# Kernel tuning notes

Hardware: AMD Instinct MI355X
Metric: run time of the kernel (lower is better)

The kernel has to match this reference:

```python
import jax, jax.numpy as jnp
import numpy as np

VOCAB = 100
EMB = 256
HID = 256
B = 8
S = 2048


def setup_inputs() -> dict:
    key = jax.random.key(0)
    ks = jax.random.split(key, 12)
    s_e = 1.0 / np.sqrt(EMB)
    s_h = 1.0 / np.sqrt(HID)
    return {
        "x": jax.random.randint(ks[0], (B, S), 0, VOCAB),
        "embedding": jax.random.normal(ks[1], (VOCAB, EMB), jnp.float32),
        "w_ih": jax.random.uniform(ks[2], (3 * HID, EMB), jnp.float32, -s_e, s_e),
        "w_hh": jax.random.uniform(ks[3], (3 * HID, HID), jnp.float32, -s_h, s_h),
        "b_ih": jax.random.uniform(ks[4], (3 * HID,), jnp.float32, -s_h, s_h),
        "b_hh": jax.random.uniform(ks[5], (3 * HID,), jnp.float32, -s_h, s_h),
        "attn_w": jax.random.uniform(ks[6], (HID, HID), jnp.float32, -s_h, s_h),
        "attn_b": jax.random.uniform(ks[7], (HID,), jnp.float32, -s_h, s_h),
        "comb_w": jax.random.uniform(ks[8], (HID, 2 * HID), jnp.float32, -s_h, s_h),
        "comb_b": jax.random.uniform(ks[9], (HID,), jnp.float32, -s_h, s_h),
        "fc_w": jax.random.uniform(ks[10], (VOCAB, HID), jnp.float32, -s_h, s_h),
        "fc_b": jax.random.uniform(ks[11], (VOCAB,), jnp.float32, -s_h, s_h),
    }


def _gru(emb, w_ih, w_hh, b_ih, b_hh):
    # emb: [B, S, E]; PyTorch GRU gate order: r, z, n
    xg = jnp.einsum('bse,ge->bsg', emb, w_ih) + b_ih  # [B, S, 3H]
    h0 = jnp.zeros((emb.shape[0], HID), emb.dtype)

    def step(h, xg_t):
        hg = h @ w_hh.T + b_hh
        xr, xz, xn = jnp.split(xg_t, 3, axis=-1)
        hr, hz, hn = jnp.split(hg, 3, axis=-1)
        r = jax.nn.sigmoid(xr + hr)
        z = jax.nn.sigmoid(xz + hz)
        n = jnp.tanh(xn + r * hn)
        h_new = (1.0 - z) * n + z * h
        return h_new, h_new

    h_last, hs = jax.lax.scan(step, h0, jnp.swapaxes(xg, 0, 1))
    return jnp.swapaxes(hs, 0, 1), h_last  # [B,S,H], [B,H]


def reference(x, embedding, w_ih, w_hh, b_ih, b_hh, attn_w, attn_b, comb_w, comb_b, fc_w, fc_b):
    emb = embedding[x]  # [B, S, E]
    all_h, h_last = _gru(emb, w_ih, w_hh, b_ih, b_hh)
    keys = jnp.einsum('bsh,kh->bsk', all_h, attn_w) + attn_b  # [B,S,H]
    scores = jnp.einsum('bqh,bkh->bqk', all_h, keys)  # [B,S,S]
    seq = all_h.shape[1]
    causal = jnp.tril(jnp.ones((seq, seq), bool))
    scores = jnp.where(causal[None], scores, -jnp.inf)
    attn = jax.nn.softmax(scores, axis=-1)
    context = jnp.einsum('bqk,bkh->bqh', attn, all_h)  # [B,S,H]
    combined = jnp.concatenate([all_h, context], axis=-1)
    combined = jnp.tanh(jnp.einsum('bsd,hd->bsh', combined, comb_w) + comb_b)
    output = jnp.einsum('bsh,vh->bsv', combined, fc_w) + fc_b
    return output, h_last[None]  # hidden: [num_layers=1, B, H]
```

## Files before the change

### kernel.cpp

```cpp
#include <hip/hip_runtime.h>

#define SEQ  2048
#define NB   8
#define HD   256
#define G3   768
#define NV   100
#define KVB  32

typedef float f32x4 __attribute__((ext_vector_type(4)));
typedef int   i32x4 __attribute__((ext_vector_type(4)));
typedef short s16x8 __attribute__((ext_vector_type(8)));
typedef unsigned short u16x4 __attribute__((ext_vector_type(4)));

#define INV26 1.490116119384765625e-8f

__device__ __forceinline__ float rcp_fast(float x) {
  return __builtin_amdgcn_rcpf(x);
}
__device__ __forceinline__ float sigm(float x) {
  x = fminf(fmaxf(x, -30.f), 30.f);
  return rcp_fast(1.f + __expf(-x));
}
__device__ __forceinline__ float tanh_fast(float x) {
  x = fminf(fmaxf(x, -15.f), 15.f);
  float e = __expf(2.f * x);
  return (e - 1.f) * rcp_fast(e + 1.f);
}
__device__ __forceinline__ void cvt_hilo(float f, unsigned short& h, unsigned short& l) {
  unsigned u = __float_as_uint(f);
  h = (unsigned short)(u >> 16);
  float r = f - __uint_as_float(u & 0xffff0000u);
  l = (unsigned short)(__float_as_uint(r) >> 16);
}

__global__ __launch_bounds__(256) void build_table(
    const float* __restrict__ emb, const float* __restrict__ w_ih,
    const float* __restrict__ b_ih, float* __restrict__ table) {
  __shared__ float eL[256];
  __shared__ float wL[256][37];
  int v = blockIdx.x, tid = threadIdx.x;
  eL[tid] = emb[v * HD + tid];
  for (int gt = 0; gt < 3; ++gt) {
    float acc = b_ih[gt * 256 + tid];
    for (int e0 = 0; e0 < HD; e0 += 32) {
      __syncthreads();
      #pragma unroll
      for (int i = 0; i < 32; ++i) {
        int idx = tid + i * 256;
        int r = idx >> 5, c = idx & 31;
        wL[r][c] = w_ih[(size_t)(gt * 256 + r) * HD + e0 + c];
      }
      __syncthreads();
      #pragma unroll
      for (int c = 0; c < 32; ++c) acc += eL[e0 + c] * wL[tid][c];
    }
    table[((size_t)v * 256 + tid) * 4 + gt] = acc;
  }
}

__global__ void __launch_bounds__(512) gru_scan(
    const int* __restrict__ x, const float* __restrict__ w_hh,
    const float* __restrict__ b_hh, const float* __restrict__ table,
    float* __restrict__ all_h, float* __restrict__ h_last) {
  __shared__ __align__(16) signed char hpk[2][2 * 272];
  __shared__ int xs[SEQ];
  const int b = blockIdx.x;
  int tid = threadIdx.x;
  int lane = tid & 63, wv = tid >> 6;
  int ncol = lane & 15, quad = lane >> 4;
  int usel = quad & 1;
  int j = wv * 32 + usel * 16 + ncol;

  for (int i = tid; i < SEQ; i += 512) xs[i] = x[b * SEQ + i];
  for (int i = tid; i < 2 * 272; i += 512)
    hpk[0][i] = (i >= 272) ? (signed char)-128 : 0;

  i32x4 bw[2][3][4];
  float Cn2[2][3];
  #pragma unroll
  for (int u = 0; u < 2; ++u) {
    #pragma unroll
    for (int t3 = 0; t3 < 3; ++t3) {
      int row = t3 * 256 + wv * 32 + u * 16 + ncol;
      int sw = 0;
      #pragma unroll
      for (int c = 0; c < 4; ++c) {
        const float* p = w_hh + (size_t)row * HD + c * 64 + quad * 16;
        unsigned pw[4] = {0u, 0u, 0u, 0u};
        #pragma unroll
        for (int e = 0; e < 16; ++e) {
          int q = __float2int_rn(p[e] * 2048.f);
          q = max(-127, min(127, q));
          sw += q;
          pw[e >> 2] |= ((unsigned)(q & 255)) << ((e & 3) * 8);
        }
        bw[u][t3][c] = (i32x4){(int)pw[0], (int)pw[1], (int)pw[2], (int)pw[3]};
      }
      sw += __shfl_xor(sw, 16);
      sw += __shfl_xor(sw, 32);
      Cn2[u][t3] = b_hh[row] + 128.f * (float)sw * INV26;
    }
  }
  float Csel[3];
  #pragma unroll
  for (int t3 = 0; t3 < 3; ++t3) Csel[t3] = usel ? Cn2[1][t3] : Cn2[0][t3];

  float hreg = 0.f;
  __syncthreads();
  float xr, xz, xn;
  {
    int v = xs[0];
    f32x4 xg = *(const f32x4*)&table[((size_t)v * 256 + j) * 4];
    xr = xg[0]; xz = xg[1]; xn = xg[2];
  }
  int a_base = (ncol & 1) * 272 + quad * 16;

  for (int t = 0; t < SEQ; ++t) {
    const signed char* cb = hpk[t & 1];
    i32x4 a[4];
    #pragma unroll
    for (int c = 0; c < 4; ++c)
      a[c] = *(const i32x4*)&cb[a_base + c * 64];
    float hg[3];
    #pragma unroll
    for (int t3 = 0; t3 < 3; ++t3) {
      i32x4 A0 = {0, 0, 0, 0}, A1 = {0, 0, 0, 0};
      #pragma unroll
      for (int c = 0; c < 4; ++c) {
        A0 = __builtin_amdgcn_mfma_i32_16x16x64_i8(a[c], bw[0][t3][c], A0, 0, 0, 0);
        A1 = __builtin_amdgcn_mfma_i32_16x16x64_i8(a[c], bw[1][t3][c], A1, 0, 0, 0);
      }
      int d0 = usel ? A1[0] : A0[0];
      int d1 = usel ? A1[1] : A0[1];
      hg[t3] = ((float)d0 * 256.f + (float)d1) * INV26 + Csel[t3];
    }
    float r = sigm(xr + hg[0]);
    float z = sigm(xz + hg[1]);
    float n = tanh_fast(xn + r * hg[2]);
    float h = (1.f - z) * n + z * hreg;
    hreg = h;
    int q = min(__float2int_rn(h * 32768.f), 32767);
    int lou = q & 255;
    int hi8 = (q - lou) >> 8;
    signed char* nx = hpk[(t + 1) & 1];
    if (quad < 2) {
      nx[j] = (signed char)hi8;
      nx[272 + j] = (signed char)(lou - 128);
      all_h[((size_t)b * SEQ + t) * HD + j] = h;
    }
    int v = xs[(t + 1 < SEQ) ? t + 1 : t];
    f32x4 xg = *(const f32x4*)&table[((size_t)v * 256 + j) * 4];
    xr = xg[0]; xz = xg[1]; xn = xg[2];
    __syncthreads();
  }
  if (quad < 2) h_last[b * HD + j] = hreg;
}

template<int ACT>
__global__ __launch_bounds__(256) void gemm_bias(
    const float* __restrict__ A, int lda,
    const float* __restrict__ W, const float* __restrict__ bias,
    float* __restrict__ C, int ldc, int N, int K) {
  __shared__ float As[128][36];
  __shared__ float Ws[64][36];
  int tid = threadIdx.x;
  int m0 = blockIdx.y * 128, n0 = blockIdx.x * 64;
  int ml = tid & 31, g = tid >> 5;
  float acc[4][8];
  #pragma unroll
  for (int i = 0; i < 4; ++i)
    #pragma unroll
    for (int jj = 0; jj < 8; ++jj) acc[i][jj] = 0.f;
  for (int k0 = 0; k0 < K; k0 += 32) {
    __syncthreads();
    #pragma unroll
    for (int i = 0; i < 4; ++i) {
      int idx = tid + i * 256;
      int r = idx >> 3, c4 = (idx & 7) * 4;
      *(f32x4*)&As[r][c4] = *(const f32x4*)&A[(size_t)(m0 + r) * lda + k0 + c4];
    }
    #pragma unroll
    for (int i = 0; i < 2; ++i) {
      int idx = tid + i * 256;
      int r = idx >> 3, c4 = (idx & 7) * 4;
      f32x4 wv = {0.f, 0.f, 0.f, 0.f};
      if (n0 + r < N) wv = *(const f32x4*)&W[(size_t)(n0 + r) * K + k0 + c4];
      *(f32x4*)&Ws[r][c4] = wv;
    }
    __syncthreads();
    #pragma unroll
    for (int k4 = 0; k4 < 32; k4 += 4) {
      f32x4 av[4], wv8[8];
      #pragma unroll
      for (int i = 0; i < 4; ++i) av[i] = *(const f32x4*)&As[ml + i * 32][k4];
      #pragma unroll
      for (int jj = 0; jj < 8; ++jj) wv8[jj] = *(const f32x4*)&Ws[g * 8 + jj][k4];
      #pragma unroll
      for (int kk = 0; kk < 4; ++kk)
        #pragma unroll
        for (int i = 0; i < 4; ++i)
          #pragma unroll
          for (int jj = 0; jj < 8; ++jj)
            acc[i][jj] += av[i][kk] * wv8[jj][kk];
    }
  }
  #pragma unroll
  for (int i = 0; i < 4; ++i) {
    int m = m0 + ml + i * 32;
    #pragma unroll
    for (int jj = 0; jj < 8; ++jj) {
      int n = n0 + g * 8 + jj;
      if (n < N) {
        float val = acc[i][jj] + bias[n];
        if (ACT) val = tanh_fast(val);
        C[(size_t)m * ldc + n] = val;
      }
    }
  }
}

__global__ __launch_bounds__(256) void gemm_bias_cat(
    const float* __restrict__ A1, const float* __restrict__ A2,
    const float* __restrict__ W, const float* __restrict__ bias,
    float* __restrict__ C) {
  __shared__ float As[128][36];
  __shared__ float Ws[64][36];
  const int K = 512;
  int tid = threadIdx.x;
  int m0 = blockIdx.y * 128, n0 = blockIdx.x * 64;
  int ml = tid & 31, g = tid >> 5;
  float acc[4][8];
  #pragma unroll
  for (int i = 0; i < 4; ++i)
    #pragma unroll
    for (int jj = 0; jj < 8; ++jj) acc[i][jj] = 0.f;
  for (int k0 = 0; k0 < K; k0 += 32) {
    const float* src = (k0 < 256) ? A1 : A2;
    int kb = (k0 < 256) ? k0 : k0 - 256;
    __syncthreads();
    #pragma unroll
    for (int i = 0; i < 4; ++i) {
      int idx = tid + i * 256;
      int r = idx >> 3, c4 = (idx & 7) * 4;
      *(f32x4*)&As[r][c4] = *(const f32x4*)&src[(size_t)(m0 + r) * 256 + kb + c4];
    }
    #pragma unroll
    for (int i = 0; i < 2; ++i) {
      int idx = tid + i * 256;
      int r = idx >> 3, c4 = (idx & 7) * 4;
      *(f32x4*)&Ws[r][c4] = *(const f32x4*)&W[(size_t)(n0 + r) * K + k0 + c4];
    }
    __syncthreads();
    #pragma unroll
    for (int k4 = 0; k4 < 32; k4 += 4) {
      f32x4 av[4], wv8[8];
      #pragma unroll
      for (int i = 0; i < 4; ++i) av[i] = *(const f32x4*)&As[ml + i * 32][k4];
      #pragma unroll
      for (int jj = 0; jj < 8; ++jj) wv8[jj] = *(const f32x4*)&Ws[g * 8 + jj][k4];
      #pragma unroll
      for (int kk = 0; kk < 4; ++kk)
        #pragma unroll
        for (int i = 0; i < 4; ++i)
          #pragma unroll
          for (int jj = 0; jj < 8; ++jj)
            acc[i][jj] += av[i][kk] * wv8[jj][kk];
    }
  }
  #pragma unroll
  for (int i = 0; i < 4; ++i) {
    int m = m0 + ml + i * 32;
    #pragma unroll
    for (int jj = 0; jj < 8; ++jj) {
      int n = n0 + g * 8 + jj;
      C[(size_t)m * 256 + n] = tanh_fast(acc[i][jj] + bias[n]);
    }
  }
}

__global__ __launch_bounds__(256, 1) void attention_kernel(
    const float* __restrict__ all_h, const float* __restrict__ keys,
    float* __restrict__ ctxg) {
  __shared__ __align__(16) unsigned short KH[2][8][516], KL[2][8][516];
  __shared__ __align__(16) unsigned short VH[16][516], VL[16][516];
  __shared__ __align__(16) unsigned short PB[4][2][520];
  const int b = blockIdx.y, qb = blockIdx.x;
  int tid = threadIdx.x, lane = tid & 63, wv = tid >> 6;
  int lm = lane & 15, kg = lane >> 4;
  const float* hb = all_h + (size_t)b * SEQ * HD;
  const float* kb = keys  + (size_t)b * SEQ * HD;
  const int q0 = qb * 64 + wv * 16;

  s16x8 Qh[8], Ql[8];
  {
    const float* qp = hb + (size_t)(q0 + lm) * HD;
    #pragma unroll
    for (int ch = 0; ch < 8; ++ch) {
      union { s16x8 v; unsigned short u[8]; } uh, ul;
      f32x4 a0 = *(const f32x4*)&qp[ch * 32 + kg * 8];
      f32x4 a1 = *(const f32x4*)&qp[ch * 32 + kg * 8 + 4];
      #pragma unroll
      for (int e = 0; e < 4; ++e) {
        cvt_hilo(a0[e], uh.u[e], ul.u[e]);
        cvt_hilo(a1[e], uh.u[4 + e], ul.u[4 + e]);
      }
      Qh[ch] = uh.v; Ql[ch] = ul.v;
    }
  }

  f32x4 co[16];
  #pragma unroll
  for (int ht = 0; ht < 16; ++ht) co[ht] = (f32x4){0.f, 0.f, 0.f, 0.f};
  float mo[4] = {-3e38f, -3e38f, -3e38f, -3e38f};
  float lr[4] = {0.f, 0.f, 0.f, 0.f};

  const int nkt = 2 * qb + 2;
  for (int kt = 0; kt < nkt; ++kt) {
    int k0 = kt * KVB;
    __syncthreads();
    #pragma unroll
    for (int i = 0; i < 8; ++i) {
      int idx = tid + i * 256;
      int r = idx >> 6, c = idx & 63;
      f32x4 kv = *(const f32x4*)&kb[(size_t)(k0 + r) * HD + c * 4];
      f32x4 vv = *(const f32x4*)&hb[(size_t)(k0 + r) * HD + c * 4];
      u16x4 khv, klv;
      #pragma unroll
      for (int e = 0; e < 4; ++e) {
        unsigned short h16, l16;
        cvt_hilo(kv[e], h16, l16);
        khv[e] = h16; klv[e] = l16;
      }
      int ch = c >> 3, kgs = (c & 7) >> 1;
      int off = (kgs * 16 + (r & 15)) * 8 + (c & 1) * 4;
      *(u16x4*)&KH[r >> 4][ch][off] = khv;
      *(u16x4*)&KL[r >> 4][ch][off] = klv;
      int kgv = r >> 3, ev = r & 7, ht = c >> 2;
      #pragma unroll
      for (int e = 0; e < 4; ++e) {
        unsigned short h16, l16;
        cvt_hilo(vv[e], h16, l16);
        int o = (kgv * 16 + (c & 3) * 4 + e) * 8 + ev;
        VH[ht][o] = h16; VL[ht][o] = l16;
      }
    }
    __syncthreads();

    float s[4][2];
    #pragma unroll
    for (int g = 0; g < 2; ++g) {
      f32x4 a0 = {0.f,0.f,0.f,0.f}, a1 = {0.f,0.f,0.f,0.f}, a2 = {0.f,0.f,0.f,0.f};
      #pragma unroll
      for (int ch = 0; ch < 8; ++ch) {
        s16x8 bh = *(const s16x8*)&KH[g][ch][lane * 8];
        s16x8 bl = *(const s16x8*)&KL[g][ch][lane * 8];
        a0 = __builtin_amdgcn_mfma_f32_16x16x32_bf16(Qh[ch], bh, a0, 0, 0, 0);
        a1 = __builtin_amdgcn_mfma_f32_16x16x32_bf16(Ql[ch], bh, a1, 0, 0, 0);
        a2 = __builtin_amdgcn_mfma_f32_16x16x32_bf16(Qh[ch], bl, a2, 0, 0, 0);
      }
      #pragma unroll
      for (int r = 0; r < 4; ++r) s[r][g] = a0[r] + a1[r] + a2[r];
    }
    float p[4][2], al[4];
    #pragma unroll
    for (int r = 0; r < 4; ++r) {
      int qrow = q0 + kg * 4 + r;
      int va = (k0 + lm) <= qrow, vb = (k0 + 16 + lm) <= qrow;
      float ta = va ? s[r][0] : -3e38f;
      float tb = vb ? s[r][1] : -3e38f;
      float t = fmaxf(ta, tb);
      t = fmaxf(t, __shfl_xor(t, 1));
      t = fmaxf(t, __shfl_xor(t, 2));
      t = fmaxf(t, __shfl_xor(t, 4));
      t = fmaxf(t, __shfl_xor(t, 8));
      float mn = fmaxf(mo[r], t);
      al[r] = __expf(mo[r] - mn);
      float pa = va ? __expf(s[r][0] - mn) : 0.f;
      float pb = vb ? __expf(s[r][1] - mn) : 0.f;
      p[r][0] = pa; p[r][1] = pb;
      float rs = pa + pb;
      rs += __shfl_xor(rs, 1);
      rs += __shfl_xor(rs, 2);
      rs += __shfl_xor(rs, 4);
      rs += __shfl_xor(rs, 8);
      lr[r] = lr[r] * al[r] + rs;
      mo[r] = mn;
    }
    #pragma unroll
    for (int r = 0; r < 4; ++r)
      #pragma unroll
      for (int g = 0; g < 2; ++g) {
        unsigned short ph, pl;
        cvt_hilo(p[r][g], ph, pl);
        int key = g * 16 + lm;
        int o = ((key >> 3) * 16 + kg * 4 + r) * 8 + (key & 7);
        PB[wv][0][o] = ph;
        PB[wv][1][o] = pl;
      }
    s16x8 pah = *(const s16x8*)&PB[wv][0][lane * 8];
    s16x8 pal = *(const s16x8*)&PB[wv][1][lane * 8];
    #pragma unroll
    for (int ht = 0; ht < 16; ++ht) {
      f32x4 c = co[ht];
      #pragma unroll
      for (int r = 0; r < 4; ++r) c[r] *= al[r];
      s16x8 vh = *(const s16x8*)&VH[ht][lane * 8];
      s16x8 vl = *(const s16x8*)&VL[ht][lane * 8];
      c = __builtin_amdgcn_mfma_f32_16x16x32_bf16(pah, vh, c, 0, 0, 0);
      c = __builtin_amdgcn_mfma_f32_16x16x32_bf16(pah, vl, c, 0, 0, 0);
      c = __builtin_amdgcn_mfma_f32_16x16x32_bf16(pal, vh, c, 0, 0, 0);
      co[ht] = c;
    }
  }
  float li[4];
  #pragma unroll
  for (int r = 0; r < 4; ++r) li[r] = rcp_fast(lr[r]);
  #pragma unroll
  for (int ht = 0; ht < 16; ++ht)
    #pragma unroll
    for (int r = 0; r < 4; ++r)
      ctxg[((size_t)b * SEQ + q0 + kg * 4 + r) * HD + ht * 16 + lm] = co[ht][r] * li[r];
}

extern "C" void kernel_launch(void* const* d_in, const int* in_sizes, int n_in,
                              void* d_out, int out_size, void* d_ws, size_t ws_size,
                              hipStream_t stream) {
  (void)in_sizes; (void)n_in; (void)out_size; (void)ws_size;
  const int*   x      = (const int*)  d_in[0];
  const float* emb    = (const float*)d_in[1];
  const float* w_ih   = (const float*)d_in[2];
  const float* w_hh   = (const float*)d_in[3];
  const float* b_ih   = (const float*)d_in[4];
  const float* b_hh   = (const float*)d_in[5];
  const float* attn_w = (const float*)d_in[6];
  const float* attn_b = (const float*)d_in[7];
  const float* comb_w = (const float*)d_in[8];
  const float* comb_b = (const float*)d_in[9];
  const float* fc_w   = (const float*)d_in[10];
  const float* fc_b   = (const float*)d_in[11];
  float* out = (float*)d_out;

  float* ws    = (float*)d_ws;
  float* table = ws;
  float* all_h = table + 102400;
  float* keys  = all_h + 4194304;
  float* ctx   = keys  + 4194304;
  float* hlast = out + (size_t)NB * SEQ * NV;

  build_table<<<100, 256, 0, stream>>>(emb, w_ih, b_ih, table);
  gru_scan<<<NB, 512, 0, stream>>>(x, w_hh, b_hh, table, all_h, hlast);
  gemm_bias<0><<<dim3(4, 128), 256, 0, stream>>>(all_h, 256, attn_w, attn_b, keys, 256, 256, 256);
  attention_kernel<<<dim3(32, 8), 256, 0, stream>>>(all_h, keys, ctx);
  gemm_bias_cat<<<dim3(4, 128), 256, 0, stream>>>(all_h, ctx, comb_w, comb_b, keys);
  gemm_bias<0><<<dim3(2, 128), 256, 0, stream>>>(keys, 256, fc_w, fc_b, out, 100, 100, 256);
}
```

Measured before the change: 1.954 ms.

## Prefetch next K/V tile into registers and defer GRU hidden-state stores

In the attention kernel, the next 32-row K/V tile is loaded from global memory into registers while the current tile's MFMAs run. This overlaps global load latency with compute, at the cost of 64 extra VGPRs per thread. The K and V shared-memory arrays get padded sub-blocks to cut LDS bank conflicts. In the sequential GRU loop, the all_h store and the next token's table gather move to the start of each step, so they overlap the MFMA chain instead of sitting before the barrier.

```diff
diff --git a/kernel.cpp b/kernel.cpp
--- a/kernel.cpp
+++ b/kernel.cpp
@@ -105,7 +105,7 @@
   #pragma unroll
   for (int t3 = 0; t3 < 3; ++t3) Csel[t3] = usel ? Cn2[1][t3] : Cn2[0][t3];
 
-  float hreg = 0.f;
+  float hreg = 0.f, hpend = 0.f;
   __syncthreads();
   float xr, xz, xn;
   {
@@ -121,6 +121,10 @@
     #pragma unroll
     for (int c = 0; c < 4; ++c)
       a[c] = *(const i32x4*)&cb[a_base + c * 64];
+    if (t > 0 && quad < 2)
+      all_h[((size_t)b * SEQ + (t - 1)) * HD + j] = hpend;
+    int vnext = xs[(t + 1 < SEQ) ? t + 1 : t];
+    f32x4 xgn = *(const f32x4*)&table[((size_t)vnext * 256 + j) * 4];
     float hg[3];
     #pragma unroll
     for (int t3 = 0; t3 < 3; ++t3) {
@@ -139,6 +143,7 @@
     float n = tanh_fast(xn + r * hg[2]);
     float h = (1.f - z) * n + z * hreg;
     hreg = h;
+    hpend = h;
     int q = min(__float2int_rn(h * 32768.f), 32767);
     int lou = q & 255;
     int hi8 = (q - lou) >> 8;
@@ -146,14 +151,14 @@
     if (quad < 2) {
       nx[j] = (signed char)hi8;
       nx[272 + j] = (signed char)(lou - 128);
-      all_h[((size_t)b * SEQ + t) * HD + j] = h;
-    }
-    int v = xs[(t + 1 < SEQ) ? t + 1 : t];
-    f32x4 xg = *(const f32x4*)&table[((size_t)v * 256 + j) * 4];
-    xr = xg[0]; xz = xg[1]; xn = xg[2];
-    __syncthreads();
-  }
-  if (quad < 2) h_last[b * HD + j] = hreg;
+    }
+    xr = xgn[0]; xz = xgn[1]; xn = xgn[2];
+    __syncthreads();
+  }
+  if (quad < 2) {
+    all_h[((size_t)b * SEQ + (SEQ - 1)) * HD + j] = hpend;
+    h_last[b * HD + j] = hreg;
+  }
 }
 
 template<int ACT>
@@ -281,8 +286,8 @@
 __global__ __launch_bounds__(256, 1) void attention_kernel(
     const float* __restrict__ all_h, const float* __restrict__ keys,
     float* __restrict__ ctxg) {
-  __shared__ __align__(16) unsigned short KH[2][8][516], KL[2][8][516];
-  __shared__ __align__(16) unsigned short VH[16][516], VL[16][516];
+  __shared__ __align__(16) unsigned short KH[2][8][4][140], KL[2][8][4][140];
+  __shared__ __align__(16) unsigned short VH[16][524], VL[16][524];
   __shared__ __align__(16) unsigned short PB[4][2][520];
   const int b = blockIdx.y, qb = blockIdx.x;
   int tid = threadIdx.x, lane = tid & 63, wv = tid >> 6;
@@ -315,15 +320,24 @@
   float lr[4] = {0.f, 0.f, 0.f, 0.f};
 
   const int nkt = 2 * qb + 2;
+  f32x4 kreg[8], vreg[8];
+  {
+    #pragma unroll
+    for (int i = 0; i < 8; ++i) {
+      int idx = tid + i * 256;
+      int r = idx >> 6, c = idx & 63;
+      kreg[i] = *(const f32x4*)&kb[(size_t)r * HD + c * 4];
+      vreg[i] = *(const f32x4*)&hb[(size_t)r * HD + c * 4];
+    }
+  }
   for (int kt = 0; kt < nkt; ++kt) {
-    int k0 = kt * KVB;
     __syncthreads();
     #pragma unroll
     for (int i = 0; i < 8; ++i) {
       int idx = tid + i * 256;
       int r = idx >> 6, c = idx & 63;
-      f32x4 kv = *(const f32x4*)&kb[(size_t)(k0 + r) * HD + c * 4];
-      f32x4 vv = *(const f32x4*)&hb[(size_t)(k0 + r) * HD + c * 4];
+      f32x4 kv = kreg[i];
+      f32x4 vv = vreg[i];
       u16x4 khv, klv;
       #pragma unroll
       for (int e = 0; e < 4; ++e) {
@@ -331,10 +345,9 @@
         cvt_hilo(kv[e], h16, l16);
         khv[e] = h16; klv[e] = l16;
       }
-      int ch = c >> 3, kgs = (c & 7) >> 1;
-      int off = (kgs * 16 + (r & 15)) * 8 + (c & 1) * 4;
-      *(u16x4*)&KH[r >> 4][ch][off] = khv;
-      *(u16x4*)&KL[r >> 4][ch][off] = klv;
+      int off = (r & 15) * 8 + (c & 1) * 4;
+      *(u16x4*)&KH[r >> 4][c >> 3][(c & 7) >> 1][off] = khv;
+      *(u16x4*)&KL[r >> 4][c >> 3][(c & 7) >> 1][off] = klv;
       int kgv = r >> 3, ev = r & 7, ht = c >> 2;
       #pragma unroll
       for (int e = 0; e < 4; ++e) {
@@ -345,6 +358,17 @@
       }
     }
     __syncthreads();
+    if (kt + 1 < nkt) {
+      int k1 = (kt + 1) * KVB;
+      #pragma unroll
+      for (int i = 0; i < 8; ++i) {
+        int idx = tid + i * 256;
+        int r = idx >> 6, c = idx & 63;
+        kreg[i] = *(const f32x4*)&kb[(size_t)(k1 + r) * HD + c * 4];
+        vreg[i] = *(const f32x4*)&hb[(size_t)(k1 + r) * HD + c * 4];
+      }
+    }
+    int k0 = kt * KVB;
 
     float s[4][2];
     #pragma unroll
@@ -352,8 +376,8 @@
       f32x4 a0 = {0.f,0.f,0.f,0.f}, a1 = {0.f,0.f,0.f,0.f}, a2 = {0.f,0.f,0.f,0.f};
       #pragma unroll
       for (int ch = 0; ch < 8; ++ch) {
-        s16x8 bh = *(const s16x8*)&KH[g][ch][lane * 8];
-        s16x8 bl = *(const s16x8*)&KL[g][ch][lane * 8];
+        s16x8 bh = *(const s16x8*)&KH[g][ch][kg][lm * 8];
+        s16x8 bl = *(const s16x8*)&KL[g][ch][kg][lm * 8];
         a0 = __builtin_amdgcn_mfma_f32_16x16x32_bf16(Qh[ch], bh, a0, 0, 0, 0);
         a1 = __builtin_amdgcn_mfma_f32_16x16x32_bf16(Ql[ch], bh, a1, 0, 0, 0);
         a2 = __builtin_amdgcn_mfma_f32_16x16x32_bf16(Qh[ch], bl, a2, 0, 0, 0);
```

After: 2.104 ms. +7.6%, slower.
